# Performance work log

Measured on AMD Instinct MI355X. Metric: run time of the kernel, lower is better.

Reference implementation:

```python
import jax, jax.numpy as jnp
import numpy as np

PAD = -10000.0
B, N, F = 512, 2048, 16
H_PHI, LAT, H_RHO = 128, 128, 128


def _xavier(key, fan_in, fan_out):
    bound = np.sqrt(6.0 / (fan_in + fan_out))
    return jax.random.uniform(key, (fan_in, fan_out), jnp.float32, -bound, bound)


def setup_inputs() -> dict:
    key = jax.random.key(0)
    ks = jax.random.split(key, 12)
    x = jax.random.normal(ks[0], (B, N, F), jnp.float32)
    # ragged set lengths: pad tail rows with -10000.0 (the module's padding sentinel)
    lengths = jax.random.randint(ks[1], (B,), 1, N + 1)
    pad_mask = jnp.arange(N)[None, :] >= lengths[:, None]  # True where padded
    x = jnp.where(pad_mask[:, :, None], PAD, x)
    params = {
        "phi_w0": _xavier(ks[2], F, H_PHI), "phi_b0": jnp.zeros((H_PHI,), jnp.float32),
        "phi_w1": _xavier(ks[3], H_PHI, H_PHI), "phi_b1": jnp.zeros((H_PHI,), jnp.float32),
        "phi_w2": _xavier(ks[4], H_PHI, H_PHI), "phi_b2": jnp.zeros((H_PHI,), jnp.float32),
        "phi_w3": _xavier(ks[5], H_PHI, LAT), "phi_b3": jnp.zeros((LAT,), jnp.float32),
        "rho_w0": _xavier(ks[6], LAT, H_RHO), "rho_b0": jnp.zeros((H_RHO,), jnp.float32),
        "rho_w1": _xavier(ks[7], H_RHO, H_RHO), "rho_b1": jnp.zeros((H_RHO,), jnp.float32),
        "rho_w2": _xavier(ks[8], H_RHO, H_RHO), "rho_b2": jnp.zeros((H_RHO,), jnp.float32),
        "rho_w3": _xavier(ks[9], H_RHO, 1), "rho_b3": jnp.zeros((1,), jnp.float32),
    }
    return {"inputs": x, **params}


def reference(inputs, phi_w0, phi_b0, phi_w1, phi_b1, phi_w2, phi_b2, phi_w3, phi_b3,
              rho_w0, rho_b0, rho_w1, rho_b1, rho_w2, rho_b2, rho_w3, rho_b3):
    b, n, f = inputs.shape
    # valid-prefix mask: sum rows before the FIRST all-(-10000) row (matches torch loop)
    is_pad = jnp.all(inputs == PAD, axis=-1)                       # [B,N]
    first = jnp.where(jnp.any(is_pad, axis=-1), jnp.argmax(is_pad, axis=-1), n)
    mask = (jnp.arange(n)[None, :] < first[:, None]).astype(inputs.dtype)  # [B,N]
    relu = jax.nn.relu
    # phi applied per point
    h = relu(inputs @ phi_w0 + phi_b0)
    h = relu(h @ phi_w1 + phi_b1)
    h = relu(h @ phi_w2 + phi_b2)
    h = relu(h @ phi_w3 + phi_b3)                                  # [B,N,LAT]
    # masked variable-length sum pooling (segment reduce)
    pooled = jnp.einsum('bnd,bn->bd', h, mask)                     # [B,LAT]
    r = relu(pooled @ rho_w0 + rho_b0)
    r = relu(r @ rho_w1 + rho_b1)
    r = relu(r @ rho_w2 + rho_b2)
    cost = (r @ rho_w3 + rho_b3)[:, 0]                             # [B]
    return cost
```

## Files before the change

### kernel.cpp

```cpp
#include <hip/hip_runtime.h>

typedef _Float16 f16;
typedef f16  f16x2  __attribute__((ext_vector_type(2)));
typedef f16  f16x8  __attribute__((ext_vector_type(8)));
typedef __fp16 h16x2 __attribute__((ext_vector_type(2)));
typedef float f32x16 __attribute__((ext_vector_type(16)));

#define B_   512
#define N_   2048
#define PADV -10000.0f

union F16x8 { f16x8 v; f16x2 h2[4]; };

__device__ __forceinline__ f16x2 pkrtz(float a, float b) {
    h16x2 r = __builtin_amdgcn_cvt_pkrtz(a, b);
    return __builtin_bit_cast(f16x2, r);
}

__global__ void prep_kernel(const float* __restrict__ w0, const float* __restrict__ w1,
                            const float* __restrict__ w2, const float* __restrict__ w3,
                            f16* __restrict__ out, float* __restrict__ pooled)
{
    int i = blockIdx.x * 256 + threadIdx.x;
    if (i < 2048) {
        out[i] = (f16)w0[(i & 15) * 128 + (i >> 4)];
    } else if (i < 51200) {
        int j = i - 2048;
        int l = j >> 14, r = j & 16383;
        int o = r >> 7, slot = r & 127;
        int s = slot >> 4, qq = (slot >> 3) & 1, jj = slot & 7;
        int sig = 32 * (s >> 1) + 16 * (s & 1) + 4 * qq + 8 * (jj >> 2) + (jj & 3);
        const float* w = (l == 0) ? w1 : (l == 1) ? w2 : w3;
        out[i] = (f16)w[sig * 128 + o];
    }
    pooled[i] = 0.f;
}

__device__ __forceinline__ int swz(int row, int chunk) {
    return row * 256 + ((chunk ^ (row & 15)) << 4);
}

__device__ __forceinline__ void gl_lds16(const void* g, void* l) {
    __builtin_amdgcn_global_load_lds(
        (const __attribute__((address_space(1))) void*)g,
        (__attribute__((address_space(3))) void*)l, 16, 0, 0);
}

__global__ __launch_bounds__(256, 2) void phi_pool_kernel(
    const float* __restrict__ x,
    const f16*  __restrict__ wtbuf,
    const float* __restrict__ pb0, const float* __restrict__ pb1,
    const float* __restrict__ pb2, const float* __restrict__ pb3,
    float* __restrict__ pooled)
{
    __shared__ f16 wA[16384];
    __shared__ f16 wB[16384];

    const int tid  = threadIdx.x;
    const int lane = tid & 63;
    const int wv   = tid >> 6;
    const int l31  = lane & 31;
    const int q    = lane >> 5;
    const int b    = blockIdx.x >> 3;
    const int p0   = (blockIdx.x & 7) * 256 + wv * 64;

    const float* xp = x + ((size_t)b * N_ + (size_t)(p0 + l31)) * 16 + 8 * q;
    float4 a0 = ((const float4*)xp)[0];
    float4 a1 = ((const float4*)xp)[1];
    float4 c0 = ((const float4*)(xp + 512))[0];
    float4 c1 = ((const float4*)(xp + 512))[1];

    f16x8 w0f[4];
    #pragma unroll
    for (int c = 0; c < 4; ++c)
        w0f[c] = *(const f16x8*)(wtbuf + (32 * c + l31) * 16 + 8 * q);

    {
        const f16* wl1 = wtbuf + 2048;
        const f16* wl2 = wtbuf + 2048 + 16384;
        #pragma unroll
        for (int i = 0; i < 8; ++i) {
            const int row   = wv * 32 + i * 4 + (lane >> 4);
            const int chunk = (lane & 15) ^ (row & 15);
            const int loff  = (wv * 32 + i * 4) * 256;
            gl_lds16(wl1 + row * 128 + chunk * 8, (char*)wA + loff);
            gl_lds16(wl2 + row * 128 + chunk * 8, (char*)wB + loff);
        }
    }

    bool vA = (a0.x != PADV) || (a0.y != PADV) || (a0.z != PADV) || (a0.w != PADV) ||
              (a1.x != PADV) || (a1.y != PADV) || (a1.z != PADV) || (a1.w != PADV);
    bool vB = (c0.x != PADV) || (c0.y != PADV) || (c0.z != PADV) || (c0.w != PADV) ||
              (c1.x != PADV) || (c1.y != PADV) || (c1.z != PADV) || (c1.w != PADV);
    unsigned long long blA = __ballot(vA), blB = __ballot(vB);
    const unsigned mA = (unsigned)blA | (unsigned)(blA >> 32);
    const unsigned mB = (unsigned)blB | (unsigned)(blB >> 32);

    F16x8 hf[2][8];
    hf[0][0].h2[0] = pkrtz(a0.x, a0.y);
    hf[0][0].h2[1] = pkrtz(a0.z, a0.w);
    hf[0][0].h2[2] = pkrtz(a1.x, a1.y);
    hf[0][0].h2[3] = pkrtz(a1.z, a1.w);
    hf[1][0].h2[0] = pkrtz(c0.x, c0.y);
    hf[1][0].h2[1] = pkrtz(c0.z, c0.w);
    hf[1][0].h2[2] = pkrtz(c1.x, c1.y);
    hf[1][0].h2[3] = pkrtz(c1.z, c1.w);

    f32x16 acc[2][4];

    #define INIT_ACC_BIAS(pb)                                              \
        {                                                                  \
            _Pragma("unroll")                                              \
            for (int c = 0; c < 4; ++c) {                                  \
                _Pragma("unroll")                                          \
                for (int g = 0; g < 4; ++g) {                              \
                    float4 bb = *(const float4*)((pb) + 32 * c + 8 * g + 4 * q); \
                    const float* bbp = (const float*)&bb;                  \
                    _Pragma("unroll")                                      \
                    for (int e = 0; e < 4; ++e) {                          \
                        acc[0][c][4 * g + e] = bbp[e];                     \
                        acc[1][c][4 * g + e] = bbp[e];                     \
                    }                                                      \
                }                                                          \
            }                                                              \
        }

    #define EPILOGUE()                                                     \
        {                                                                  \
            const f16x2 z2 = {(f16)0.f, (f16)0.f};                         \
            _Pragma("unroll")                                              \
            for (int t = 0; t < 2; ++t) {                                  \
                _Pragma("unroll")                                          \
                for (int s = 0; s < 8; ++s) {                              \
                    const int c = s >> 1, r0 = 8 * (s & 1);                \
                    _Pragma("unroll")                                      \
                    for (int p = 0; p < 4; ++p) {                          \
                        f16x2 m = pkrtz(                                   \
                            acc[t][c][r0 + 2 * p], acc[t][c][r0 + 2 * p + 1]); \
                        hf[t][s].h2[p] = __builtin_elementwise_max(m, z2); \
                    }                                                      \
                }                                                          \
            }                                                              \
        }

    INIT_ACC_BIAS(pb0);
    #pragma unroll
    for (int c = 0; c < 4; ++c) {
        acc[0][c] = __builtin_amdgcn_mfma_f32_32x32x16_f16(w0f[c], hf[0][0].v, acc[0][c], 0, 0, 0);
        acc[1][c] = __builtin_amdgcn_mfma_f32_32x32x16_f16(w0f[c], hf[1][0].v, acc[1][c], 0, 0, 0);
    }
    EPILOGUE();

    __syncthreads();

    INIT_ACC_BIAS(pb1);
    #pragma unroll
    for (int s = 0; s < 8; ++s) {
        f16x8 wf[4];
        #pragma unroll
        for (int c = 0; c < 4; ++c)
            wf[c] = *(const f16x8*)((const char*)wA + swz(32 * c + l31, 2 * s + q));
        #pragma unroll
        for (int c = 0; c < 4; ++c) {
            acc[0][c] = __builtin_amdgcn_mfma_f32_32x32x16_f16(wf[c], hf[0][s].v, acc[0][c], 0, 0, 0);
            acc[1][c] = __builtin_amdgcn_mfma_f32_32x32x16_f16(wf[c], hf[1][s].v, acc[1][c], 0, 0, 0);
        }
    }

    __syncthreads();

    {
        const f16* wl3 = wtbuf + 2048 + 32768;
        #pragma unroll
        for (int i = 0; i < 8; ++i) {
            const int row   = wv * 32 + i * 4 + (lane >> 4);
            const int chunk = (lane & 15) ^ (row & 15);
            const int loff  = (wv * 32 + i * 4) * 256;
            gl_lds16(wl3 + row * 128 + chunk * 8, (char*)wA + loff);
        }
    }

    EPILOGUE();

    INIT_ACC_BIAS(pb2);
    #pragma unroll
    for (int s = 0; s < 8; ++s) {
        f16x8 wf[4];
        #pragma unroll
        for (int c = 0; c < 4; ++c)
            wf[c] = *(const f16x8*)((const char*)wB + swz(32 * c + l31, 2 * s + q));
        #pragma unroll
        for (int c = 0; c < 4; ++c) {
            acc[0][c] = __builtin_amdgcn_mfma_f32_32x32x16_f16(wf[c], hf[0][s].v, acc[0][c], 0, 0, 0);
            acc[1][c] = __builtin_amdgcn_mfma_f32_32x32x16_f16(wf[c], hf[1][s].v, acc[1][c], 0, 0, 0);
        }
    }
    EPILOGUE();

    __syncthreads();

    {
        float bL[4];
        #pragma unroll
        for (int c = 0; c < 4; ++c) bL[c] = pb3[32 * c + l31];
        #pragma unroll
        for (int t = 0; t < 2; ++t)
            #pragma unroll
            for (int c = 0; c < 4; ++c)
                #pragma unroll
                for (int r = 0; r < 16; ++r) acc[t][c][r] = bL[c];
    }
    #pragma unroll
    for (int s = 0; s < 8; ++s) {
        f16x8 wf[4];
        #pragma unroll
        for (int c = 0; c < 4; ++c)
            wf[c] = *(const f16x8*)((const char*)wA + swz(32 * c + l31, 2 * s + q));
        #pragma unroll
        for (int c = 0; c < 4; ++c) {
            acc[0][c] = __builtin_amdgcn_mfma_f32_32x32x16_f16(hf[0][s].v, wf[c], acc[0][c], 0, 0, 0);
            acc[1][c] = __builtin_amdgcn_mfma_f32_32x32x16_f16(hf[1][s].v, wf[c], acc[1][c], 0, 0, 0);
        }
    }

    #pragma unroll
    for (int c = 0; c < 4; ++c) {
        float s0 = 0.f;
        #pragma unroll
        for (int t = 0; t < 2; ++t) {
            const unsigned m = t ? mB : mA;
            #pragma unroll
            for (int r = 0; r < 16; ++r) {
                const int ptl = 4 * q + (r & 3) + 8 * (r >> 2);
                float v = fmaxf(acc[t][c][r], 0.f);
                s0 += ((m >> ptl) & 1u) ? v : 0.f;
            }
        }
        s0 += __shfl_xor(s0, 32);
        if (q == 0) atomicAdd(&pooled[b * 128 + 32 * c + l31], s0);
    }
}

__global__ __launch_bounds__(128) void rho_kernel(
    const float* __restrict__ pooled,
    const float* __restrict__ w0, const float* __restrict__ b0,
    const float* __restrict__ w1, const float* __restrict__ b1,
    const float* __restrict__ w2, const float* __restrict__ b2,
    const float* __restrict__ w3, const float* __restrict__ b3,
    float* __restrict__ out)
{
    __shared__ float buf[2][128];
    __shared__ float red[2];
    const int b = blockIdx.x, t = threadIdx.x;
    buf[0][t] = pooled[b * 128 + t];
    __syncthreads();
    const float* ws3[3] = {w0, w1, w2};
    const float* bs3[3] = {b0, b1, b2};
    int cur = 0;
    #pragma unroll 1
    for (int l = 0; l < 3; ++l) {
        float acc = bs3[l][t];
        const float* w = ws3[l];
        #pragma unroll 8
        for (int k = 0; k < 128; ++k)
            acc = fmaf(buf[cur][k], w[k * 128 + t], acc);
        buf[cur ^ 1][t] = fmaxf(acc, 0.f);
        cur ^= 1;
        __syncthreads();
    }
    float v = buf[cur][t] * w3[t];
    #pragma unroll
    for (int off = 32; off > 0; off >>= 1)
        v += __shfl_down(v, off, 64);
    if ((t & 63) == 0) red[t >> 6] = v;
    __syncthreads();
    if (t == 0) out[b] = red[0] + red[1] + b3[0];
}

extern "C" void kernel_launch(void* const* d_in, const int* in_sizes, int n_in,
                              void* d_out, int out_size, void* d_ws, size_t ws_size,
                              hipStream_t stream)
{
    (void)in_sizes; (void)n_in; (void)out_size; (void)ws_size;
    const float* x      = (const float*)d_in[0];
    const float* phi_w0 = (const float*)d_in[1];
    const float* phi_b0 = (const float*)d_in[2];
    const float* phi_w1 = (const float*)d_in[3];
    const float* phi_b1 = (const float*)d_in[4];
    const float* phi_w2 = (const float*)d_in[5];
    const float* phi_b2 = (const float*)d_in[6];
    const float* phi_w3 = (const float*)d_in[7];
    const float* phi_b3 = (const float*)d_in[8];
    const float* rho_w0 = (const float*)d_in[9];
    const float* rho_b0 = (const float*)d_in[10];
    const float* rho_w1 = (const float*)d_in[11];
    const float* rho_b1 = (const float*)d_in[12];
    const float* rho_w2 = (const float*)d_in[13];
    const float* rho_b2 = (const float*)d_in[14];
    const float* rho_w3 = (const float*)d_in[15];
    const float* rho_b3 = (const float*)d_in[16];

    float* pooled = (float*)d_ws;
    f16*   wtbuf  = (f16*)((char*)d_ws + 262144);

    prep_kernel<<<256, 256, 0, stream>>>(phi_w0, phi_w1, phi_w2, phi_w3, wtbuf, pooled);
    phi_pool_kernel<<<4096, 256, 0, stream>>>(x, wtbuf, phi_b0, phi_b1, phi_b2, phi_b3, pooled);
    rho_kernel<<<B_, 128, 0, stream>>>(pooled, rho_w0, rho_b0, rho_w1, rho_b1,
                                       rho_w2, rho_b2, rho_w3, rho_b3, (float*)d_out);
}
```

Before: 226.0 us.

## Fuse phi, pooling and rho into one kernel with padded-tile early exit

Replaces the per-tile phi kernel and the separate rho kernel with one kernel of 256 blocks. Each block handles two batch rows, and each wave loops over 64-row tiles, stopping at the first tile that is entirely padding. The W1 and W2 layer weights are loaded into LDS once per block. The W3 weights are pre-permuted into MFMA fragment order and read straight from global memory. The last wave to finish a batch row, found with an atomic counter, runs the rho MLP, which removes a kernel launch and skips work on padded tail rows. The trade-offs are far fewer blocks with possible load imbalance across ragged lengths, plus serial per-wave tile loops.

```diff
diff --git a/kernel.cpp b/kernel.cpp
--- a/kernel.cpp
+++ b/kernel.cpp
@@ -19,21 +19,33 @@
 
 __global__ void prep_kernel(const float* __restrict__ w0, const float* __restrict__ w1,
                             const float* __restrict__ w2, const float* __restrict__ w3,
-                            f16* __restrict__ out, float* __restrict__ pooled)
+                            f16* __restrict__ wt, float* __restrict__ pooled,
+                            int* __restrict__ cnt)
 {
     int i = blockIdx.x * 256 + threadIdx.x;
     if (i < 2048) {
-        out[i] = (f16)w0[(i & 15) * 128 + (i >> 4)];
-    } else if (i < 51200) {
+        wt[i] = (f16)w0[(i & 15) * 128 + (i >> 4)];
+    } else if (i < 34816) {
         int j = i - 2048;
         int l = j >> 14, r = j & 16383;
         int o = r >> 7, slot = r & 127;
         int s = slot >> 4, qq = (slot >> 3) & 1, jj = slot & 7;
         int sig = 32 * (s >> 1) + 16 * (s & 1) + 4 * qq + 8 * (jj >> 2) + (jj & 3);
-        const float* w = (l == 0) ? w1 : (l == 1) ? w2 : w3;
-        out[i] = (f16)w[sig * 128 + o];
-    }
-    pooled[i] = 0.f;
+        const float* w = (l == 0) ? w1 : w2;
+        wt[i] = (f16)w[sig * 128 + o];
+    } else if (i < 51200) {
+        int k = i - 34816;
+        int jj = k & 7;
+        int lane = (k >> 3) & 63;
+        int sc = k >> 9;
+        int s = sc >> 2, c = sc & 3;
+        int l31 = lane & 31, qq = lane >> 5;
+        int row = 32 * c + l31;
+        int sig = 32 * (s >> 1) + 16 * (s & 1) + 4 * qq + 8 * (jj >> 2) + (jj & 3);
+        wt[i] = (f16)w3[sig * 128 + row];
+    }
+    pooled[i & 65535] = 0.f;
+    if (i < 512) cnt[i] = 0;
 }
 
 __device__ __forceinline__ int swz(int row, int chunk) {
@@ -46,80 +58,75 @@
         (__attribute__((address_space(3))) void*)l, 16, 0, 0);
 }
 
-__global__ __launch_bounds__(256, 2) void phi_pool_kernel(
-    const float* __restrict__ x,
-    const f16*  __restrict__ wtbuf,
+__global__ __launch_bounds__(512, 2) void deepset_kernel(
+    const float* __restrict__ x, const f16* __restrict__ wtbuf,
+    float* __restrict__ pooled, int* __restrict__ cntG,
     const float* __restrict__ pb0, const float* __restrict__ pb1,
     const float* __restrict__ pb2, const float* __restrict__ pb3,
-    float* __restrict__ pooled)
+    const float* __restrict__ rw0, const float* __restrict__ rb0,
+    const float* __restrict__ rw1, const float* __restrict__ rb1,
+    const float* __restrict__ rw2, const float* __restrict__ rb2,
+    const float* __restrict__ rw3, const float* __restrict__ rb3,
+    float* __restrict__ out)
 {
-    __shared__ f16 wA[16384];
-    __shared__ f16 wB[16384];
+    __shared__ f16 wAll[32768];
 
     const int tid  = threadIdx.x;
     const int lane = tid & 63;
     const int wv   = tid >> 6;
     const int l31  = lane & 31;
     const int q    = lane >> 5;
-    const int b    = blockIdx.x >> 3;
-    const int p0   = (blockIdx.x & 7) * 256 + wv * 64;
-
-    const float* xp = x + ((size_t)b * N_ + (size_t)(p0 + l31)) * 16 + 8 * q;
-    float4 a0 = ((const float4*)xp)[0];
-    float4 a1 = ((const float4*)xp)[1];
-    float4 c0 = ((const float4*)(xp + 512))[0];
-    float4 c1 = ((const float4*)(xp + 512))[1];
+    const int half = wv >> 2;
+    const int w4   = wv & 3;
+    const int bb   = blockIdx.x * 2 + half;
+
+    {
+        const f16* wsrc = wtbuf + 2048;
+        #pragma unroll
+        for (int i = 0; i < 8; ++i) {
+            const int row   = wv * 32 + i * 4 + (lane >> 4);
+            const int chunk = (lane & 15) ^ (row & 15);
+            const int loff  = (wv * 32 + i * 4) * 256;
+            gl_lds16(wsrc + row * 128 + chunk * 8, (char*)wAll + loff);
+        }
+    }
 
     f16x8 w0f[4];
     #pragma unroll
     for (int c = 0; c < 4; ++c)
         w0f[c] = *(const f16x8*)(wtbuf + (32 * c + l31) * 16 + 8 * q);
-
+    float bL[4];
+    #pragma unroll
+    for (int c = 0; c < 4; ++c) bL[c] = pb3[32 * c + l31];
+
+    const f16* w3x = wtbuf + 34816;
+
+    const size_t rowb = (size_t)bb * N_;
+    float4 na0, na1, nc0, nc1;
     {
-        const f16* wl1 = wtbuf + 2048;
-        const f16* wl2 = wtbuf + 2048 + 16384;
-        #pragma unroll
-        for (int i = 0; i < 8; ++i) {
-            const int row   = wv * 32 + i * 4 + (lane >> 4);
-            const int chunk = (lane & 15) ^ (row & 15);
-            const int loff  = (wv * 32 + i * 4) * 256;
-            gl_lds16(wl1 + row * 128 + chunk * 8, (char*)wA + loff);
-            gl_lds16(wl2 + row * 128 + chunk * 8, (char*)wB + loff);
-        }
-    }
-
-    bool vA = (a0.x != PADV) || (a0.y != PADV) || (a0.z != PADV) || (a0.w != PADV) ||
-              (a1.x != PADV) || (a1.y != PADV) || (a1.z != PADV) || (a1.w != PADV);
-    bool vB = (c0.x != PADV) || (c0.y != PADV) || (c0.z != PADV) || (c0.w != PADV) ||
-              (c1.x != PADV) || (c1.y != PADV) || (c1.z != PADV) || (c1.w != PADV);
-    unsigned long long blA = __ballot(vA), blB = __ballot(vB);
-    const unsigned mA = (unsigned)blA | (unsigned)(blA >> 32);
-    const unsigned mB = (unsigned)blB | (unsigned)(blB >> 32);
-
+        const float* xg = x + (rowb + (size_t)(64 * w4 + l31)) * 16 + 8 * q;
+        na0 = ((const float4*)xg)[0];
+        na1 = ((const float4*)xg)[1];
+        nc0 = ((const float4*)(xg + 512))[0];
+        nc1 = ((const float4*)(xg + 512))[1];
+    }
+
+    float sums[4] = {0.f, 0.f, 0.f, 0.f};
+    f32x16 acc[2][4];
     F16x8 hf[2][8];
-    hf[0][0].h2[0] = pkrtz(a0.x, a0.y);
-    hf[0][0].h2[1] = pkrtz(a0.z, a0.w);
-    hf[0][0].h2[2] = pkrtz(a1.x, a1.y);
-    hf[0][0].h2[3] = pkrtz(a1.z, a1.w);
-    hf[1][0].h2[0] = pkrtz(c0.x, c0.y);
-    hf[1][0].h2[1] = pkrtz(c0.z, c0.w);
-    hf[1][0].h2[2] = pkrtz(c1.x, c1.y);
-    hf[1][0].h2[3] = pkrtz(c1.z, c1.w);
-
-    f32x16 acc[2][4];
 
     #define INIT_ACC_BIAS(pb)                                              \
         {                                                                  \
             _Pragma("unroll")                                              \
             for (int c = 0; c < 4; ++c) {                                  \
                 _Pragma("unroll")                                          \
-                for (int g = 0; g < 4; ++g) {                              \
-                    float4 bb = *(const float4*)((pb) + 32 * c + 8 * g + 4 * q); \
-                    const float* bbp = (const float*)&bb;                  \
+                for (int g2 = 0; g2 < 4; ++g2) {                           \
+                    float4 bbv = *(const float4*)((pb) + 32 * c + 8 * g2 + 4 * q); \
+                    const float* bbp = (const float*)&bbv;                 \
                     _Pragma("unroll")                                      \
                     for (int e = 0; e < 4; ++e) {                          \
-                        acc[0][c][4 * g + e] = bbp[e];                     \
-                        acc[1][c][4 * g + e] = bbp[e];                     \
+                        acc[0][c][4 * g2 + e] = bbp[e];                    \
+                        acc[1][c][4 * g2 + e] = bbp[e];                    \
                     }                                                      \
                 }                                                          \
             }                                                              \
@@ -143,138 +150,156 @@
             }                                                              \
         }
 
-    INIT_ACC_BIAS(pb0);
-    #pragma unroll
-    for (int c = 0; c < 4; ++c) {
-        acc[0][c] = __builtin_amdgcn_mfma_f32_32x32x16_f16(w0f[c], hf[0][0].v, acc[0][c], 0, 0, 0);
-        acc[1][c] = __builtin_amdgcn_mfma_f32_32x32x16_f16(w0f[c], hf[1][0].v, acc[1][c], 0, 0, 0);
-    }
-    EPILOGUE();
-
     __syncthreads();
 
-    INIT_ACC_BIAS(pb1);
-    #pragma unroll
-    for (int s = 0; s < 8; ++s) {
-        f16x8 wf[4];
-        #pragma unroll
-        for (int c = 0; c < 4; ++c)
-            wf[c] = *(const f16x8*)((const char*)wA + swz(32 * c + l31, 2 * s + q));
+    #pragma unroll 1
+    for (int g = 0; g < 8; ++g) {
+        const float4 a0 = na0, a1 = na1, c0 = nc0, c1 = nc1;
+
+        bool vA = (a0.x != PADV) || (a0.y != PADV) || (a0.z != PADV) || (a0.w != PADV) ||
+                  (a1.x != PADV) || (a1.y != PADV) || (a1.z != PADV) || (a1.w != PADV);
+        bool vB = (c0.x != PADV) || (c0.y != PADV) || (c0.z != PADV) || (c0.w != PADV) ||
+                  (c1.x != PADV) || (c1.y != PADV) || (c1.z != PADV) || (c1.w != PADV);
+        unsigned long long blA = __ballot(vA), blB = __ballot(vB);
+        const unsigned mA = (unsigned)blA | (unsigned)(blA >> 32);
+        const unsigned mB = (unsigned)blB | (unsigned)(blB >> 32);
+        if ((mA | mB) == 0u) break;
+
+        hf[0][0].h2[0] = pkrtz(a0.x, a0.y);
+        hf[0][0].h2[1] = pkrtz(a0.z, a0.w);
+        hf[0][0].h2[2] = pkrtz(a1.x, a1.y);
+        hf[0][0].h2[3] = pkrtz(a1.z, a1.w);
+        hf[1][0].h2[0] = pkrtz(c0.x, c0.y);
+        hf[1][0].h2[1] = pkrtz(c0.z, c0.w);
+        hf[1][0].h2[2] = pkrtz(c1.x, c1.y);
+        hf[1][0].h2[3] = pkrtz(c1.z, c1.w);
+
+        {
+            const int gn = (g < 7) ? g + 1 : 7;
+            const float* xg = x + (rowb + (size_t)(64 * (w4 + 4 * gn) + l31)) * 16 + 8 * q;
+            na0 = ((const float4*)xg)[0];
+            na1 = ((const float4*)xg)[1];
+            nc0 = ((const float4*)(xg + 512))[0];
+            nc1 = ((const float4*)(xg + 512))[1];
+        }
+
+        INIT_ACC_BIAS(pb0);
         #pragma unroll
         for (int c = 0; c < 4; ++c) {
-            acc[0][c] = __builtin_amdgcn_mfma_f32_32x32x16_f16(wf[c], hf[0][s].v, acc[0][c], 0, 0, 0);
-            acc[1][c] = __builtin_amdgcn_mfma_f32_32x32x16_f16(wf[c], hf[1][s].v, acc[1][c], 0, 0, 0);
-        }
-    }
-
-    __syncthreads();
-
-    {
-        const f16* wl3 = wtbuf + 2048 + 32768;
-        #pragma unroll
-        for (int i = 0; i < 8; ++i) {
-            const int row   = wv * 32 + i * 4 + (lane >> 4);
-            const int chunk = (lane & 15) ^ (row & 15);
-            const int loff  = (wv * 32 + i * 4) * 256;
-            gl_lds16(wl3 + row * 128 + chunk * 8, (char*)wA + loff);
-        }
-    }
-
-    EPILOGUE();
-
-    INIT_ACC_BIAS(pb2);
-    #pragma unroll
-    for (int s = 0; s < 8; ++s) {
-        f16x8 wf[4];
-        #pragma unroll
-        for (int c = 0; c < 4; ++c)
-            wf[c] = *(const f16x8*)((const char*)wB + swz(32 * c + l31, 2 * s + q));
-        #pragma unroll
-        for (int c = 0; c < 4; ++c) {
-            acc[0][c] = __builtin_amdgcn_mfma_f32_32x32x16_f16(wf[c], hf[0][s].v, acc[0][c], 0, 0, 0);
-            acc[1][c] = __builtin_amdgcn_mfma_f32_32x32x16_f16(wf[c], hf[1][s].v, acc[1][c], 0, 0, 0);
-        }
-    }
-    EPILOGUE();
-
-    __syncthreads();
-
-    {
-        float bL[4];
-        #pragma unroll
-        for (int c = 0; c < 4; ++c) bL[c] = pb3[32 * c + l31];
+            acc[0][c] = __builtin_amdgcn_mfma_f32_32x32x16_f16(w0f[c], hf[0][0].v, acc[0][c], 0, 0, 0);
+            acc[1][c] = __builtin_amdgcn_mfma_f32_32x32x16_f16(w0f[c], hf[1][0].v, acc[1][c], 0, 0, 0);
+        }
+        EPILOGUE();
+
+        INIT_ACC_BIAS(pb1);
+        #pragma unroll
+        for (int s = 0; s < 8; ++s) {
+            f16x8 wf[4];
+            #pragma unroll
+            for (int c = 0; c < 4; ++c)
+                wf[c] = *(const f16x8*)((const char*)wAll + swz(32 * c + l31, 2 * s + q));
+            #pragma unroll
+            for (int c = 0; c < 4; ++c) {
+                acc[0][c] = __builtin_amdgcn_mfma_f32_32x32x16_f16(wf[c], hf[0][s].v, acc[0][c], 0, 0, 0);
+                acc[1][c] = __builtin_amdgcn_mfma_f32_32x32x16_f16(wf[c], hf[1][s].v, acc[1][c], 0, 0, 0);
+            }
+        }
+        EPILOGUE();
+
+        INIT_ACC_BIAS(pb2);
+        #pragma unroll
+        for (int s = 0; s < 8; ++s) {
+            f16x8 wf[4];
+            #pragma unroll
+            for (int c = 0; c < 4; ++c)
+                wf[c] = *(const f16x8*)((const char*)wAll + 32768 + swz(32 * c + l31, 2 * s + q));
+            #pragma unroll
+            for (int c = 0; c < 4; ++c) {
+                acc[0][c] = __builtin_amdgcn_mfma_f32_32x32x16_f16(wf[c], hf[0][s].v, acc[0][c], 0, 0, 0);
+                acc[1][c] = __builtin_amdgcn_mfma_f32_32x32x16_f16(wf[c], hf[1][s].v, acc[1][c], 0, 0, 0);
+            }
+        }
+        EPILOGUE();
+
         #pragma unroll
         for (int t = 0; t < 2; ++t)
             #pragma unroll
             for (int c = 0; c < 4; ++c)
                 #pragma unroll
                 for (int r = 0; r < 16; ++r) acc[t][c][r] = bL[c];
-    }
-    #pragma unroll
-    for (int s = 0; s < 8; ++s) {
-        f16x8 wf[4];
-        #pragma unroll
-        for (int c = 0; c < 4; ++c)
-            wf[c] = *(const f16x8*)((const char*)wA + swz(32 * c + l31, 2 * s + q));
+        #pragma unroll
+        for (int s = 0; s < 8; ++s) {
+            f16x8 wf[4];
+            #pragma unroll
+            for (int c = 0; c < 4; ++c)
+                wf[c] = *(const f16x8*)(w3x + ((s * 4 + c) * 64 + lane) * 8);
+            #pragma unroll
+            for (int c = 0; c < 4; ++c) {
+                acc[0][c] = __builtin_amdgcn_mfma_f32_32x32x16_f16(hf[0][s].v, wf[c], acc[0][c], 0, 0, 0);
+                acc[1][c] = __builtin_amdgcn_mfma_f32_32x32x16_f16(hf[1][s].v, wf[c], acc[1][c], 0, 0, 0);
+            }
+        }
+
         #pragma unroll
         for (int c = 0; c < 4; ++c) {
-            acc[0][c] = __builtin_amdgcn_mfma_f32_32x32x16_f16(hf[0][s].v, wf[c], acc[0][c], 0, 0, 0);
-            acc[1][c] = __builtin_amdgcn_mfma_f32_32x32x16_f16(hf[1][s].v, wf[c], acc[1][c], 0, 0, 0);
+            float s0 = 0.f;
+            #pragma unroll
+            for (int t = 0; t < 2; ++t) {
+                const unsigned m = t ? mB : mA;
+                #pragma unroll
+                for (int r = 0; r < 16; ++r) {
+                    const int ptl = 4 * q + (r & 3) + 8 * (r >> 2);
+                    float v = fmaxf(acc[t][c][r], 0.f);
+                    s0 += ((m >> ptl) & 1u) ? v : 0.f;
+                }
+            }
+            sums[c] += s0;
         }
     }
 
     #pragma unroll
     for (int c = 0; c < 4; ++c) {
-        float s0 = 0.f;
-        #pragma unroll
-        for (int t = 0; t < 2; ++t) {
-            const unsigned m = t ? mB : mA;
-            #pragma unroll
-            for (int r = 0; r < 16; ++r) {
-                const int ptl = 4 * q + (r & 3) + 8 * (r >> 2);
-                float v = fmaxf(acc[t][c][r], 0.f);
-                s0 += ((m >> ptl) & 1u) ? v : 0.f;
-            }
-        }
+        float s0 = sums[c];
         s0 += __shfl_xor(s0, 32);
-        if (q == 0) atomicAdd(&pooled[b * 128 + 32 * c + l31], s0);
-    }
-}
-
-__global__ __launch_bounds__(128) void rho_kernel(
-    const float* __restrict__ pooled,
-    const float* __restrict__ w0, const float* __restrict__ b0,
-    const float* __restrict__ w1, const float* __restrict__ b1,
-    const float* __restrict__ w2, const float* __restrict__ b2,
-    const float* __restrict__ w3, const float* __restrict__ b3,
-    float* __restrict__ out)
-{
-    __shared__ float buf[2][128];
-    __shared__ float red[2];
-    const int b = blockIdx.x, t = threadIdx.x;
-    buf[0][t] = pooled[b * 128 + t];
-    __syncthreads();
-    const float* ws3[3] = {w0, w1, w2};
-    const float* bs3[3] = {b0, b1, b2};
-    int cur = 0;
-    #pragma unroll 1
-    for (int l = 0; l < 3; ++l) {
-        float acc = bs3[l][t];
-        const float* w = ws3[l];
-        #pragma unroll 8
-        for (int k = 0; k < 128; ++k)
-            acc = fmaf(buf[cur][k], w[k * 128 + t], acc);
-        buf[cur ^ 1][t] = fmaxf(acc, 0.f);
-        cur ^= 1;
-        __syncthreads();
-    }
-    float v = buf[cur][t] * w3[t];
-    #pragma unroll
-    for (int off = 32; off > 0; off >>= 1)
-        v += __shfl_down(v, off, 64);
-    if ((t & 63) == 0) red[t >> 6] = v;
-    __syncthreads();
-    if (t == 0) out[b] = red[0] + red[1] + b3[0];
+        if (q == 0) atomicAdd(&pooled[bb * 128 + 32 * c + l31], s0);
+    }
+    __threadfence();
+
+    int old = 0;
+    if (lane == 0) old = atomicAdd(&cntG[bb], 1);
+    old = __shfl(old, 0);
+    if (old == 3) {
+        __threadfence();
+        float p0 = atomicAdd(&pooled[bb * 128 + lane], 0.f);
+        float p1 = atomicAdd(&pooled[bb * 128 + 64 + lane], 0.f);
+        const float* rws[3] = {rw0, rw1, rw2};
+        const float* rbs[3] = {rb0, rb1, rb2};
+        #pragma unroll 1
+        for (int l = 0; l < 3; ++l) {
+            const float* w = rws[l];
+            float acc0 = rbs[l][lane];
+            float acc1 = rbs[l][64 + lane];
+            #pragma unroll 8
+            for (int k = 0; k < 64; ++k) {
+                float pk = __shfl(p0, k);
+                acc0 = fmaf(pk, w[k * 128 + lane], acc0);
+                acc1 = fmaf(pk, w[k * 128 + 64 + lane], acc1);
+            }
+            #pragma unroll 8
+            for (int k = 0; k < 64; ++k) {
+                float pk = __shfl(p1, k);
+                acc0 = fmaf(pk, w[(k + 64) * 128 + lane], acc0);
+                acc1 = fmaf(pk, w[(k + 64) * 128 + 64 + lane], acc1);
+            }
+            p0 = fmaxf(acc0, 0.f);
+            p1 = fmaxf(acc1, 0.f);
+        }
+        float v = p0 * rw3[lane] + p1 * rw3[64 + lane];
+        #pragma unroll
+        for (int off = 32; off > 0; off >>= 1)
+            v += __shfl_down(v, off, 64);
+        if (lane == 0) out[bb] = v + rb3[0];
+    }
 }
 
 extern "C" void kernel_launch(void* const* d_in, const int* in_sizes, int n_in,
@@ -301,10 +326,14 @@
     const float* rho_b3 = (const float*)d_in[16];
 
     float* pooled = (float*)d_ws;
-    f16*   wtbuf  = (f16*)((char*)d_ws + 262144);
-
-    prep_kernel<<<256, 256, 0, stream>>>(phi_w0, phi_w1, phi_w2, phi_w3, wtbuf, pooled);
-    phi_pool_kernel<<<4096, 256, 0, stream>>>(x, wtbuf, phi_b0, phi_b1, phi_b2, phi_b3, pooled);
-    rho_kernel<<<B_, 128, 0, stream>>>(pooled, rho_w0, rho_b0, rho_w1, rho_b1,
-                                       rho_w2, rho_b2, rho_w3, rho_b3, (float*)d_out);
-}
+    int*   cntG   = (int*)((char*)d_ws + 262144);
+    f16*   wtbuf  = (f16*)((char*)d_ws + 262144 + 2048);
+
+    prep_kernel<<<256, 256, 0, stream>>>(phi_w0, phi_w1, phi_w2, phi_w3,
+                                         wtbuf, pooled, cntG);
+    deepset_kernel<<<256, 512, 0, stream>>>(x, wtbuf, pooled, cntG,
+                                            phi_b0, phi_b1, phi_b2, phi_b3,
+                                            rho_w0, rho_b0, rho_w1, rho_b1,
+                                            rho_w2, rho_b2, rho_w3, rho_b3,
+                                            (float*)d_out);
+}
```

New measurement: 380.9 us. 68.5% more time.

## Persistent wave-level work queue that skips fully padded tiles and prefetches inputs

Applied to the files above, without the earlier changes.

Turns the phi kernel into a persistent kernel with 512 blocks. Each wave takes 64-point tiles from a global atomic counter and loads the next tile's inputs while it computes the current one. Tiles where every row is padding are skipped, so the four MLP layers run only where points can contribute. W3 is pre-arranged into per-lane MFMA fragment order and read straight from global memory instead of LDS. This removes the mid-kernel LDS reload and its barriers, but adds atomic-queue traffic and more global/L2 reads of W3 on every tile.

```diff
diff --git a/kernel.cpp b/kernel.cpp
--- a/kernel.cpp
+++ b/kernel.cpp
@@ -19,21 +19,33 @@
 
 __global__ void prep_kernel(const float* __restrict__ w0, const float* __restrict__ w1,
                             const float* __restrict__ w2, const float* __restrict__ w3,
-                            f16* __restrict__ out, float* __restrict__ pooled)
+                            f16* __restrict__ wt, float* __restrict__ pooled,
+                            int* __restrict__ qhead)
 {
     int i = blockIdx.x * 256 + threadIdx.x;
     if (i < 2048) {
-        out[i] = (f16)w0[(i & 15) * 128 + (i >> 4)];
-    } else if (i < 51200) {
+        wt[i] = (f16)w0[(i & 15) * 128 + (i >> 4)];
+    } else if (i < 34816) {
         int j = i - 2048;
         int l = j >> 14, r = j & 16383;
         int o = r >> 7, slot = r & 127;
         int s = slot >> 4, qq = (slot >> 3) & 1, jj = slot & 7;
         int sig = 32 * (s >> 1) + 16 * (s & 1) + 4 * qq + 8 * (jj >> 2) + (jj & 3);
-        const float* w = (l == 0) ? w1 : (l == 1) ? w2 : w3;
-        out[i] = (f16)w[sig * 128 + o];
+        const float* w = (l == 0) ? w1 : w2;
+        wt[i] = (f16)w[sig * 128 + o];
+    } else if (i < 51200) {
+        int k = i - 34816;
+        int jj = k & 7;
+        int lane = (k >> 3) & 63;
+        int sc = k >> 9;
+        int s = sc >> 2, c = sc & 3;
+        int l31 = lane & 31, qq = lane >> 5;
+        int row = 32 * c + l31;
+        int sig = 32 * (s >> 1) + 16 * (s & 1) + 4 * qq + 8 * (jj >> 2) + (jj & 3);
+        wt[i] = (f16)w3[sig * 128 + row];
     }
     pooled[i] = 0.f;
+    if (i == 0) *qhead = 0;
 }
 
 __device__ __forceinline__ int swz(int row, int chunk) {
@@ -49,9 +61,9 @@
 __global__ __launch_bounds__(256, 2) void phi_pool_kernel(
     const float* __restrict__ x,
     const f16*  __restrict__ wtbuf,
+    float* __restrict__ pooled, int* __restrict__ qhead,
     const float* __restrict__ pb0, const float* __restrict__ pb1,
-    const float* __restrict__ pb2, const float* __restrict__ pb3,
-    float* __restrict__ pooled)
+    const float* __restrict__ pb2, const float* __restrict__ pb3)
 {
     __shared__ f16 wA[16384];
     __shared__ f16 wB[16384];
@@ -61,19 +73,6 @@
     const int wv   = tid >> 6;
     const int l31  = lane & 31;
     const int q    = lane >> 5;
-    const int b    = blockIdx.x >> 3;
-    const int p0   = (blockIdx.x & 7) * 256 + wv * 64;
-
-    const float* xp = x + ((size_t)b * N_ + (size_t)(p0 + l31)) * 16 + 8 * q;
-    float4 a0 = ((const float4*)xp)[0];
-    float4 a1 = ((const float4*)xp)[1];
-    float4 c0 = ((const float4*)(xp + 512))[0];
-    float4 c1 = ((const float4*)(xp + 512))[1];
-
-    f16x8 w0f[4];
-    #pragma unroll
-    for (int c = 0; c < 4; ++c)
-        w0f[c] = *(const f16x8*)(wtbuf + (32 * c + l31) * 16 + 8 * q);
 
     {
         const f16* wl1 = wtbuf + 2048;
@@ -88,38 +87,45 @@
         }
     }
 
-    bool vA = (a0.x != PADV) || (a0.y != PADV) || (a0.z != PADV) || (a0.w != PADV) ||
-              (a1.x != PADV) || (a1.y != PADV) || (a1.z != PADV) || (a1.w != PADV);
-    bool vB = (c0.x != PADV) || (c0.y != PADV) || (c0.z != PADV) || (c0.w != PADV) ||
-              (c1.x != PADV) || (c1.y != PADV) || (c1.z != PADV) || (c1.w != PADV);
-    unsigned long long blA = __ballot(vA), blB = __ballot(vB);
-    const unsigned mA = (unsigned)blA | (unsigned)(blA >> 32);
-    const unsigned mB = (unsigned)blB | (unsigned)(blB >> 32);
-
+    f16x8 w0f[4];
+    #pragma unroll
+    for (int c = 0; c < 4; ++c)
+        w0f[c] = *(const f16x8*)(wtbuf + (32 * c + l31) * 16 + 8 * q);
+    float bL[4];
+    #pragma unroll
+    for (int c = 0; c < 4; ++c) bL[c] = pb3[32 * c + l31];
+    const f16* w3x = wtbuf + 34816;
+
+    __syncthreads();
+
+    int j;
+    if (lane == 0) j = atomicAdd(qhead, 1);
+    j = __shfl(j, 0);
+    bool have = (j < 16384);
+    float4 a0, a1, c0, c1;
+    if (have) {
+        const float* xg = x + ((size_t)(j >> 5) * N_ + (size_t)((j & 31) * 64 + l31)) * 16 + 8 * q;
+        a0 = ((const float4*)xg)[0];
+        a1 = ((const float4*)xg)[1];
+        c0 = ((const float4*)(xg + 512))[0];
+        c1 = ((const float4*)(xg + 512))[1];
+    }
+
+    f32x16 acc[2][4];
     F16x8 hf[2][8];
-    hf[0][0].h2[0] = pkrtz(a0.x, a0.y);
-    hf[0][0].h2[1] = pkrtz(a0.z, a0.w);
-    hf[0][0].h2[2] = pkrtz(a1.x, a1.y);
-    hf[0][0].h2[3] = pkrtz(a1.z, a1.w);
-    hf[1][0].h2[0] = pkrtz(c0.x, c0.y);
-    hf[1][0].h2[1] = pkrtz(c0.z, c0.w);
-    hf[1][0].h2[2] = pkrtz(c1.x, c1.y);
-    hf[1][0].h2[3] = pkrtz(c1.z, c1.w);
-
-    f32x16 acc[2][4];
 
     #define INIT_ACC_BIAS(pb)                                              \
         {                                                                  \
             _Pragma("unroll")                                              \
             for (int c = 0; c < 4; ++c) {                                  \
                 _Pragma("unroll")                                          \
-                for (int g = 0; g < 4; ++g) {                              \
-                    float4 bb = *(const float4*)((pb) + 32 * c + 8 * g + 4 * q); \
-                    const float* bbp = (const float*)&bb;                  \
+                for (int g2 = 0; g2 < 4; ++g2) {                           \
+                    float4 bbv = *(const float4*)((pb) + 32 * c + 8 * g2 + 4 * q); \
+                    const float* bbp = (const float*)&bbv;                 \
                     _Pragma("unroll")                                      \
                     for (int e = 0; e < 4; ++e) {                          \
-                        acc[0][c][4 * g + e] = bbp[e];                     \
-                        acc[1][c][4 * g + e] = bbp[e];                     \
+                        acc[0][c][4 * g2 + e] = bbp[e];                    \
+                        acc[1][c][4 * g2 + e] = bbp[e];                    \
                     }                                                      \
                 }                                                          \
             }                                                              \
@@ -143,101 +149,116 @@
             }                                                              \
         }
 
-    INIT_ACC_BIAS(pb0);
-    #pragma unroll
-    for (int c = 0; c < 4; ++c) {
-        acc[0][c] = __builtin_amdgcn_mfma_f32_32x32x16_f16(w0f[c], hf[0][0].v, acc[0][c], 0, 0, 0);
-        acc[1][c] = __builtin_amdgcn_mfma_f32_32x32x16_f16(w0f[c], hf[1][0].v, acc[1][c], 0, 0, 0);
-    }
-    EPILOGUE();
-
-    __syncthreads();
-
-    INIT_ACC_BIAS(pb1);
-    #pragma unroll
-    for (int s = 0; s < 8; ++s) {
-        f16x8 wf[4];
-        #pragma unroll
-        for (int c = 0; c < 4; ++c)
-            wf[c] = *(const f16x8*)((const char*)wA + swz(32 * c + l31, 2 * s + q));
-        #pragma unroll
-        for (int c = 0; c < 4; ++c) {
-            acc[0][c] = __builtin_amdgcn_mfma_f32_32x32x16_f16(wf[c], hf[0][s].v, acc[0][c], 0, 0, 0);
-            acc[1][c] = __builtin_amdgcn_mfma_f32_32x32x16_f16(wf[c], hf[1][s].v, acc[1][c], 0, 0, 0);
-        }
-    }
-
-    __syncthreads();
-
-    {
-        const f16* wl3 = wtbuf + 2048 + 32768;
-        #pragma unroll
-        for (int i = 0; i < 8; ++i) {
-            const int row   = wv * 32 + i * 4 + (lane >> 4);
-            const int chunk = (lane & 15) ^ (row & 15);
-            const int loff  = (wv * 32 + i * 4) * 256;
-            gl_lds16(wl3 + row * 128 + chunk * 8, (char*)wA + loff);
-        }
-    }
-
-    EPILOGUE();
-
-    INIT_ACC_BIAS(pb2);
-    #pragma unroll
-    for (int s = 0; s < 8; ++s) {
-        f16x8 wf[4];
-        #pragma unroll
-        for (int c = 0; c < 4; ++c)
-            wf[c] = *(const f16x8*)((const char*)wB + swz(32 * c + l31, 2 * s + q));
-        #pragma unroll
-        for (int c = 0; c < 4; ++c) {
-            acc[0][c] = __builtin_amdgcn_mfma_f32_32x32x16_f16(wf[c], hf[0][s].v, acc[0][c], 0, 0, 0);
-            acc[1][c] = __builtin_amdgcn_mfma_f32_32x32x16_f16(wf[c], hf[1][s].v, acc[1][c], 0, 0, 0);
-        }
-    }
-    EPILOGUE();
-
-    __syncthreads();
-
-    {
-        float bL[4];
-        #pragma unroll
-        for (int c = 0; c < 4; ++c) bL[c] = pb3[32 * c + l31];
-        #pragma unroll
-        for (int t = 0; t < 2; ++t)
-            #pragma unroll
-            for (int c = 0; c < 4; ++c)
-                #pragma unroll
-                for (int r = 0; r < 16; ++r) acc[t][c][r] = bL[c];
-    }
-    #pragma unroll
-    for (int s = 0; s < 8; ++s) {
-        f16x8 wf[4];
-        #pragma unroll
-        for (int c = 0; c < 4; ++c)
-            wf[c] = *(const f16x8*)((const char*)wA + swz(32 * c + l31, 2 * s + q));
-        #pragma unroll
-        for (int c = 0; c < 4; ++c) {
-            acc[0][c] = __builtin_amdgcn_mfma_f32_32x32x16_f16(hf[0][s].v, wf[c], acc[0][c], 0, 0, 0);
-            acc[1][c] = __builtin_amdgcn_mfma_f32_32x32x16_f16(hf[1][s].v, wf[c], acc[1][c], 0, 0, 0);
-        }
-    }
-
-    #pragma unroll
-    for (int c = 0; c < 4; ++c) {
-        float s0 = 0.f;
-        #pragma unroll
-        for (int t = 0; t < 2; ++t) {
-            const unsigned m = t ? mB : mA;
-            #pragma unroll
-            for (int r = 0; r < 16; ++r) {
-                const int ptl = 4 * q + (r & 3) + 8 * (r >> 2);
-                float v = fmaxf(acc[t][c][r], 0.f);
-                s0 += ((m >> ptl) & 1u) ? v : 0.f;
-            }
-        }
-        s0 += __shfl_xor(s0, 32);
-        if (q == 0) atomicAdd(&pooled[b * 128 + 32 * c + l31], s0);
+    #pragma unroll 1
+    while (have) {
+        const int bcur = j >> 5;
+
+        bool vA = (a0.x != PADV) || (a0.y != PADV) || (a0.z != PADV) || (a0.w != PADV) ||
+                  (a1.x != PADV) || (a1.y != PADV) || (a1.z != PADV) || (a1.w != PADV);
+        bool vB = (c0.x != PADV) || (c0.y != PADV) || (c0.z != PADV) || (c0.w != PADV) ||
+                  (c1.x != PADV) || (c1.y != PADV) || (c1.z != PADV) || (c1.w != PADV);
+        unsigned long long blA = __ballot(vA), blB = __ballot(vB);
+        const unsigned mA = (unsigned)blA | (unsigned)(blA >> 32);
+        const unsigned mB = (unsigned)blB | (unsigned)(blB >> 32);
+        const bool live = (mA | mB) != 0u;
+
+        hf[0][0].h2[0] = pkrtz(a0.x, a0.y);
+        hf[0][0].h2[1] = pkrtz(a0.z, a0.w);
+        hf[0][0].h2[2] = pkrtz(a1.x, a1.y);
+        hf[0][0].h2[3] = pkrtz(a1.z, a1.w);
+        hf[1][0].h2[0] = pkrtz(c0.x, c0.y);
+        hf[1][0].h2[1] = pkrtz(c0.z, c0.w);
+        hf[1][0].h2[2] = pkrtz(c1.x, c1.y);
+        hf[1][0].h2[3] = pkrtz(c1.z, c1.w);
+
+        if (lane == 0) j = atomicAdd(qhead, 1);
+        j = __shfl(j, 0);
+        const bool haveN = (j < 16384);
+        if (haveN) {
+            const float* xg = x + ((size_t)(j >> 5) * N_ + (size_t)((j & 31) * 64 + l31)) * 16 + 8 * q;
+            a0 = ((const float4*)xg)[0];
+            a1 = ((const float4*)xg)[1];
+            c0 = ((const float4*)(xg + 512))[0];
+            c1 = ((const float4*)(xg + 512))[1];
+        }
+
+        if (live) {
+            INIT_ACC_BIAS(pb0);
+            #pragma unroll
+            for (int c = 0; c < 4; ++c) {
+                acc[0][c] = __builtin_amdgcn_mfma_f32_32x32x16_f16(w0f[c], hf[0][0].v, acc[0][c], 0, 0, 0);
+                acc[1][c] = __builtin_amdgcn_mfma_f32_32x32x16_f16(w0f[c], hf[1][0].v, acc[1][c], 0, 0, 0);
+            }
+            EPILOGUE();
+
+            INIT_ACC_BIAS(pb1);
+            #pragma unroll
+            for (int s = 0; s < 8; ++s) {
+                f16x8 wf[4];
+                #pragma unroll
+                for (int c = 0; c < 4; ++c)
+                    wf[c] = *(const f16x8*)((const char*)wA + swz(32 * c + l31, 2 * s + q));
+                #pragma unroll
+                for (int c = 0; c < 4; ++c) {
+                    acc[0][c] = __builtin_amdgcn_mfma_f32_32x32x16_f16(wf[c], hf[0][s].v, acc[0][c], 0, 0, 0);
+                    acc[1][c] = __builtin_amdgcn_mfma_f32_32x32x16_f16(wf[c], hf[1][s].v, acc[1][c], 0, 0, 0);
+                }
+            }
+            EPILOGUE();
+
+            INIT_ACC_BIAS(pb2);
+            #pragma unroll
+            for (int s = 0; s < 8; ++s) {
+                f16x8 wf[4];
+                #pragma unroll
+                for (int c = 0; c < 4; ++c)
+                    wf[c] = *(const f16x8*)((const char*)wB + swz(32 * c + l31, 2 * s + q));
+                #pragma unroll
+                for (int c = 0; c < 4; ++c) {
+                    acc[0][c] = __builtin_amdgcn_mfma_f32_32x32x16_f16(wf[c], hf[0][s].v, acc[0][c], 0, 0, 0);
+                    acc[1][c] = __builtin_amdgcn_mfma_f32_32x32x16_f16(wf[c], hf[1][s].v, acc[1][c], 0, 0, 0);
+                }
+            }
+            EPILOGUE();
+
+            #pragma unroll
+            for (int t = 0; t < 2; ++t)
+                #pragma unroll
+                for (int c = 0; c < 4; ++c)
+                    #pragma unroll
+                    for (int r = 0; r < 16; ++r) acc[t][c][r] = bL[c];
+            #pragma unroll
+            for (int s = 0; s < 8; ++s) {
+                f16x8 wf[4];
+                #pragma unroll
+                for (int c = 0; c < 4; ++c)
+                    wf[c] = *(const f16x8*)(w3x + ((s * 4 + c) * 64 + lane) * 8);
+                #pragma unroll
+                for (int c = 0; c < 4; ++c) {
+                    acc[0][c] = __builtin_amdgcn_mfma_f32_32x32x16_f16(hf[0][s].v, wf[c], acc[0][c], 0, 0, 0);
+                    acc[1][c] = __builtin_amdgcn_mfma_f32_32x32x16_f16(hf[1][s].v, wf[c], acc[1][c], 0, 0, 0);
+                }
+            }
+
+            #pragma unroll
+            for (int c = 0; c < 4; ++c) {
+                float s0 = 0.f;
+                #pragma unroll
+                for (int t = 0; t < 2; ++t) {
+                    const unsigned m = t ? mB : mA;
+                    #pragma unroll
+                    for (int r = 0; r < 16; ++r) {
+                        const int ptl = 4 * q + (r & 3) + 8 * (r >> 2);
+                        float v = fmaxf(acc[t][c][r], 0.f);
+                        s0 += ((m >> ptl) & 1u) ? v : 0.f;
+                    }
+                }
+                s0 += __shfl_xor(s0, 32);
+                if (q == 0) atomicAdd(&pooled[bcur * 128 + 32 * c + l31], s0);
+            }
+        }
+
+        have = haveN;
     }
 }
 
@@ -301,10 +322,13 @@
     const float* rho_b3 = (const float*)d_in[16];
 
     float* pooled = (float*)d_ws;
-    f16*   wtbuf  = (f16*)((char*)d_ws + 262144);
-
-    prep_kernel<<<256, 256, 0, stream>>>(phi_w0, phi_w1, phi_w2, phi_w3, wtbuf, pooled);
-    phi_pool_kernel<<<4096, 256, 0, stream>>>(x, wtbuf, phi_b0, phi_b1, phi_b2, phi_b3, pooled);
+    int*   qhead  = (int*)((char*)d_ws + 262144);
+    f16*   wtbuf  = (f16*)((char*)d_ws + 262144 + 2048);
+
+    prep_kernel<<<256, 256, 0, stream>>>(phi_w0, phi_w1, phi_w2, phi_w3,
+                                         wtbuf, pooled, qhead);
+    phi_pool_kernel<<<512, 256, 0, stream>>>(x, wtbuf, pooled, qhead,
+                                             phi_b0, phi_b1, phi_b2, phi_b3);
     rho_kernel<<<B_, 128, 0, stream>>>(pooled, rho_w0, rho_b0, rho_w1, rho_b1,
                                        rho_w2, rho_b2, rho_w3, rho_b3, (float*)d_out);
 }
```

Measured after the change: 380.0 us. +68.1%, slower.
